# Optimization experiments

Hardware: AMD Instinct MI355X
Metric: run time of the kernel (lower is better)

The kernel has to match this reference:

```python
import jax, jax.numpy as jnp
import numpy as np

B, D, N = 65536, 512, 1024  # batch, latent_dim, som_dim**2


def setup_inputs() -> dict:
    key = jax.random.key(0)
    k1, k2, k3, k4, k5 = jax.random.split(key, 5)
    return {
        "x": jax.random.normal(k1, (B, D), dtype=jnp.float32),
        "W": jax.random.normal(k2, (D, D), dtype=jnp.float32) * 0.02,
        "b": jax.random.normal(k3, (D,), dtype=jnp.float32) * 0.02,
        "prototypes": jax.random.normal(k4, (N, D), dtype=jnp.float32),
        "temp_raw": jnp.array([0.5], dtype=jnp.float32),
    }


def reference(x, W, b, prototypes, temp_raw):
    # encoder_fc: Linear(latent_dim, latent_dim)
    z = x @ W.T + b  # [B, D]
    # torch.cdist (p=2) via ||z||^2 + ||p||^2 - 2 z.p, avoids [B,N,D] intermediate
    z_sq = jnp.sum(z * z, axis=-1, keepdims=True)          # [B, 1]
    p_sq = jnp.sum(prototypes * prototypes, axis=-1)        # [N]
    d2 = jnp.maximum(z_sq + p_sq - 2.0 * (z @ prototypes.T), 1e-12)
    dists = jnp.sqrt(d2)                                    # [B, N]
    # temperature = sigmoid(temp_raw) * (1 - 0.001) + 0.001
    temp = jax.nn.sigmoid(temp_raw[0]) * (1.0 - 0.001) + 0.001
    weights = jax.nn.softmax(-dists / temp, axis=-1)        # [B, N]
    blended = weights @ prototypes                          # [B, D]
    return blended, weights
```

## Files before the change

kernel.cpp:

```cpp
#include <hip/hip_runtime.h>

#define DDIM 512
#define NPROT 1024

typedef float fvec4 __attribute__((ext_vector_type(4)));
typedef __bf16 bf16x8 __attribute__((ext_vector_type(8)));
typedef unsigned short us4 __attribute__((ext_vector_type(4)));
typedef unsigned short us8 __attribute__((ext_vector_type(8)));
typedef __attribute__((address_space(1))) unsigned int gu32;
typedef __attribute__((address_space(3))) unsigned int lu32;

__device__ __forceinline__ unsigned short f2bf(float f) {
  unsigned u = __float_as_uint(f);
  u += 0x7fffu + ((u >> 16) & 1u);
  return (unsigned short)(u >> 16);
}
__device__ __forceinline__ float bf2f(unsigned short h) {
  return __uint_as_float(((unsigned)h) << 16);
}
__device__ __forceinline__ void gl_lds16(const void* g, void* l) {
  __builtin_amdgcn_global_load_lds((gu32*)(unsigned long long)g,
                                   (lu32*)(unsigned)(unsigned long long)l,
                                   16, 0, 0);
}

__global__ __launch_bounds__(256) void prep_kernel(
    const float* __restrict__ W, const float* __restrict__ P,
    unsigned short* __restrict__ Wb, unsigned short* __restrict__ Pb,
    unsigned short* __restrict__ PTb, float* __restrict__ psq) {
  __shared__ float tile[32][33];
  const int b = blockIdx.x;
  const int t = threadIdx.x;
  if (b < 256) {
    int e = (b * 256 + t) * 4;
    fvec4 v = *(const fvec4*)(W + e);
    us4 o; o.x = f2bf(v.x); o.y = f2bf(v.y); o.z = f2bf(v.z); o.w = f2bf(v.w);
    *(us4*)(Wb + e) = o;
  } else if (b < 768) {
    int e = ((b - 256) * 256 + t) * 4;
    fvec4 v = *(const fvec4*)(P + e);
    us4 o; o.x = f2bf(v.x); o.y = f2bf(v.y); o.z = f2bf(v.z); o.w = f2bf(v.w);
    *(us4*)(Pb + e) = o;
  } else if (b < 1280) {
    int rel = b - 768;
    int d0 = (rel >> 5) * 32;
    int n0 = (rel & 31) * 32;
    int r = t >> 3;
    int c4 = (t & 7) * 4;
    fvec4 v = *(const fvec4*)(P + (size_t)(n0 + r) * DDIM + d0 + c4);
    tile[r][c4 + 0] = v.x; tile[r][c4 + 1] = v.y;
    tile[r][c4 + 2] = v.z; tile[r][c4 + 3] = v.w;
    __syncthreads();
    us4 o;
    o.x = f2bf(tile[c4 + 0][r]);
    o.y = f2bf(tile[c4 + 1][r]);
    o.z = f2bf(tile[c4 + 2][r]);
    o.w = f2bf(tile[c4 + 3][r]);
    *(us4*)(PTb + (size_t)(d0 + r) * NPROT + n0 + c4) = o;
  } else {
    int l = t & 63;
    int row = (b - 1280) * 4 + (t >> 6);
    const float* pr = P + (size_t)row * DDIM;
    fvec4 a = *(const fvec4*)(pr + l * 4);
    fvec4 c = *(const fvec4*)(pr + 256 + l * 4);
    float s = a.x * a.x + a.y * a.y + a.z * a.z + a.w * a.w +
              c.x * c.x + c.y * c.y + c.z * c.z + c.w * c.w;
    for (int o = 32; o > 0; o >>= 1) s += __shfl_xor(s, o);
    if (l == 0) psq[row] = s;
  }
}

__global__ __launch_bounds__(256) void g1_kernel(
    const float* __restrict__ x, const unsigned short* __restrict__ Wb,
    const float* __restrict__ bias, unsigned short* __restrict__ z) {
  __shared__ unsigned short Ab[128 * 32];
  __shared__ unsigned short Bb[128 * 32];
  const int t = threadIdx.x;
  const int bm = blockIdx.x, bn = blockIdx.y;
  const int w = t >> 6, l = t & 63, lr = l & 15, lq = l >> 4;
  const int wm = (w >> 1) * 64, wn = (w & 1) * 64;
  fvec4 acc[4][4];
#pragma unroll
  for (int r = 0; r < 4; r++)
#pragma unroll
    for (int c = 0; c < 4; c++) acc[r][c] = 0.0f;
  const float* Ag = x + (size_t)bm * 128 * DDIM;
  const unsigned short* Bg = Wb + (size_t)bn * 128 * DDIM;
  for (int k0 = 0; k0 < DDIM; k0 += 32) {
    __syncthreads();
#pragma unroll
    for (int i = 0; i < 2; i++) {
      int c = i * 256 + t;
      gl_lds16(Bg + (size_t)(c >> 2) * DDIM + k0 + (c & 3) * 8, Bb + c * 8);
    }
#pragma unroll
    for (int i = 0; i < 4; i++) {
      int c = i * 256 + t;
      int row = c >> 3, j = (c & 7) * 4;
      fvec4 v = *(const fvec4*)(Ag + (size_t)row * DDIM + k0 + j);
      us4 o; o.x = f2bf(v.x); o.y = f2bf(v.y); o.z = f2bf(v.z); o.w = f2bf(v.w);
      *(us4*)(Ab + row * 32 + j) = o;
    }
    __syncthreads();
    bf16x8 af[4], bfr[4];
#pragma unroll
    for (int r = 0; r < 4; r++)
      af[r] = *(const bf16x8*)(Ab + (wm + r * 16 + lr) * 32 + lq * 8);
#pragma unroll
    for (int c = 0; c < 4; c++)
      bfr[c] = *(const bf16x8*)(Bb + (wn + c * 16 + lr) * 32 + lq * 8);
#pragma unroll
    for (int r = 0; r < 4; r++)
#pragma unroll
      for (int c = 0; c < 4; c++)
        acc[r][c] = __builtin_amdgcn_mfma_f32_16x16x32_bf16(af[r], bfr[c], acc[r][c], 0, 0, 0);
  }
  const int rbase = bm * 128 + wm + lq * 4;
  const int cbase = bn * 128 + wn + lr;
#pragma unroll
  for (int c = 0; c < 4; c++) {
    int col = cbase + c * 16;
    float bc = bias[col];
#pragma unroll
    for (int r = 0; r < 4; r++) {
      int row = rbase + r * 16;
#pragma unroll
      for (int v = 0; v < 4; v++)
        z[(size_t)(row + v) * DDIM + col] = f2bf(acc[r][c][v] + bc);
    }
  }
}

__global__ __launch_bounds__(256) void zsq_kernel(
    const unsigned short* __restrict__ z, float* __restrict__ zsq) {
  const int t = threadIdx.x, l = t & 63;
  const size_t row = (size_t)blockIdx.x * 4 + (t >> 6);
  us8 u = *(const us8*)(z + row * DDIM + l * 8);
  float s = 0.f;
#pragma unroll
  for (int i = 0; i < 8; i++) { float f = bf2f(u[i]); s += f * f; }
  for (int o = 32; o > 0; o >>= 1) s += __shfl_xor(s, o);
  if (l == 0) zsq[row] = s;
}

__global__ __launch_bounds__(256) void g2_kernel(
    const unsigned short* __restrict__ z, const unsigned short* __restrict__ Pb,
    const float* __restrict__ zsq, const float* __restrict__ psq,
    const float* __restrict__ temp_raw, float* __restrict__ logits) {
  __shared__ unsigned short Ab[128 * 32];
  __shared__ unsigned short Bb[128 * 32];
  const int t = threadIdx.x;
  const int bm = blockIdx.x, bn = blockIdx.y;
  const int w = t >> 6, l = t & 63, lr = l & 15, lq = l >> 4;
  const int wm = (w >> 1) * 64, wn = (w & 1) * 64;
  fvec4 acc[4][4];
#pragma unroll
  for (int r = 0; r < 4; r++)
#pragma unroll
    for (int c = 0; c < 4; c++) acc[r][c] = 0.0f;
  const unsigned short* Ag = z + (size_t)bm * 128 * DDIM;
  const unsigned short* Bg = Pb + (size_t)bn * 128 * DDIM;
  for (int k0 = 0; k0 < DDIM; k0 += 32) {
    __syncthreads();
#pragma unroll
    for (int i = 0; i < 2; i++) {
      int c = i * 256 + t;
      gl_lds16(Ag + (size_t)(c >> 2) * DDIM + k0 + (c & 3) * 8, Ab + c * 8);
      gl_lds16(Bg + (size_t)(c >> 2) * DDIM + k0 + (c & 3) * 8, Bb + c * 8);
    }
    __syncthreads();
    bf16x8 af[4], bfr[4];
#pragma unroll
    for (int r = 0; r < 4; r++)
      af[r] = *(const bf16x8*)(Ab + (wm + r * 16 + lr) * 32 + lq * 8);
#pragma unroll
    for (int c = 0; c < 4; c++)
      bfr[c] = *(const bf16x8*)(Bb + (wn + c * 16 + lr) * 32 + lq * 8);
#pragma unroll
    for (int r = 0; r < 4; r++)
#pragma unroll
      for (int c = 0; c < 4; c++)
        acc[r][c] = __builtin_amdgcn_mfma_f32_16x16x32_bf16(af[r], bfr[c], acc[r][c], 0, 0, 0);
  }
  const float temp = 0.999f / (1.0f + __expf(-temp_raw[0])) + 0.001f;
  const float nit = -1.0f / temp;
  const int rbase = bm * 128 + wm + lq * 4;
  const int cbase = bn * 128 + wn + lr;
  float zr[4][4];
#pragma unroll
  for (int r = 0; r < 4; r++)
#pragma unroll
    for (int v = 0; v < 4; v++) zr[r][v] = zsq[rbase + r * 16 + v];
#pragma unroll
  for (int c = 0; c < 4; c++) {
    int col = cbase + c * 16;
    float pc = psq[col];
#pragma unroll
    for (int r = 0; r < 4; r++)
#pragma unroll
      for (int v = 0; v < 4; v++) {
        float d2 = fmaxf(zr[r][v] + pc - 2.0f * acc[r][c][v], 1e-12f);
        logits[(size_t)(rbase + r * 16 + v) * NPROT + col] = nit * sqrtf(d2);
      }
  }
}

__global__ __launch_bounds__(256) void softmax_kernel(float* __restrict__ wio) {
  const int t = threadIdx.x, l = t & 63;
  float* p = wio + ((size_t)blockIdx.x * 4 + (t >> 6)) * NPROT;
  fvec4 v[4];
#pragma unroll
  for (int j = 0; j < 4; j++) v[j] = *(const fvec4*)(p + (j * 64 + l) * 4);
  float m = -3.4e38f;
#pragma unroll
  for (int j = 0; j < 4; j++)
    m = fmaxf(m, fmaxf(fmaxf(v[j].x, v[j].y), fmaxf(v[j].z, v[j].w)));
  for (int o = 32; o > 0; o >>= 1) m = fmaxf(m, __shfl_xor(m, o));
  float s = 0.f;
#pragma unroll
  for (int j = 0; j < 4; j++) {
    v[j].x = __expf(v[j].x - m); v[j].y = __expf(v[j].y - m);
    v[j].z = __expf(v[j].z - m); v[j].w = __expf(v[j].w - m);
    s += v[j].x + v[j].y + v[j].z + v[j].w;
  }
  for (int o = 32; o > 0; o >>= 1) s += __shfl_xor(s, o);
  const float rinv = 1.0f / s;
#pragma unroll
  for (int j = 0; j < 4; j++) {
    v[j] *= rinv;
    *(fvec4*)(p + (j * 64 + l) * 4) = v[j];
  }
}

__global__ __launch_bounds__(256) void g3_kernel(
    const float* __restrict__ wgt, const unsigned short* __restrict__ PTb,
    float* __restrict__ blended) {
  __shared__ unsigned short Ab[128 * 32];
  __shared__ unsigned short Bb[128 * 32];
  const int t = threadIdx.x;
  const int bm = blockIdx.x, bn = blockIdx.y;
  const int w = t >> 6, l = t & 63, lr = l & 15, lq = l >> 4;
  const int wm = (w >> 1) * 64, wn = (w & 1) * 64;
  fvec4 acc[4][4];
#pragma unroll
  for (int r = 0; r < 4; r++)
#pragma unroll
    for (int c = 0; c < 4; c++) acc[r][c] = 0.0f;
  const float* Ag = wgt + (size_t)bm * 128 * NPROT;
  const unsigned short* Bg = PTb + (size_t)bn * 128 * NPROT;
  for (int k0 = 0; k0 < NPROT; k0 += 32) {
    __syncthreads();
#pragma unroll
    for (int i = 0; i < 2; i++) {
      int c = i * 256 + t;
      gl_lds16(Bg + (size_t)(c >> 2) * NPROT + k0 + (c & 3) * 8, Bb + c * 8);
    }
#pragma unroll
    for (int i = 0; i < 4; i++) {
      int c = i * 256 + t;
      int row = c >> 3, j = (c & 7) * 4;
      fvec4 v = *(const fvec4*)(Ag + (size_t)row * NPROT + k0 + j);
      us4 o; o.x = f2bf(v.x); o.y = f2bf(v.y); o.z = f2bf(v.z); o.w = f2bf(v.w);
      *(us4*)(Ab + row * 32 + j) = o;
    }
    __syncthreads();
    bf16x8 af[4], bfr[4];
#pragma unroll
    for (int r = 0; r < 4; r++)
      af[r] = *(const bf16x8*)(Ab + (wm + r * 16 + lr) * 32 + lq * 8);
#pragma unroll
    for (int c = 0; c < 4; c++)
      bfr[c] = *(const bf16x8*)(Bb + (wn + c * 16 + lr) * 32 + lq * 8);
#pragma unroll
    for (int r = 0; r < 4; r++)
#pragma unroll
      for (int c = 0; c < 4; c++)
        acc[r][c] = __builtin_amdgcn_mfma_f32_16x16x32_bf16(af[r], bfr[c], acc[r][c], 0, 0, 0);
  }
  const int rbase = bm * 128 + wm + lq * 4;
  const int cbase = bn * 128 + wn + lr;
#pragma unroll
  for (int c = 0; c < 4; c++) {
    int col = cbase + c * 16;
#pragma unroll
    for (int r = 0; r < 4; r++) {
      int row = rbase + r * 16;
#pragma unroll
      for (int v = 0; v < 4; v++)
        blended[(size_t)(row + v) * DDIM + col] = acc[r][c][v];
    }
  }
}

extern "C" void kernel_launch(void* const* d_in, const int* in_sizes, int n_in,
                              void* d_out, int out_size, void* d_ws, size_t ws_size,
                              hipStream_t stream) {
  (void)in_sizes; (void)n_in; (void)out_size; (void)ws_size;
  const float* x  = (const float*)d_in[0];
  const float* W  = (const float*)d_in[1];
  const float* bv = (const float*)d_in[2];
  const float* P  = (const float*)d_in[3];
  const float* tr = (const float*)d_in[4];

  float* out = (float*)d_out;
  float* blended = out;
  float* weights = out + (size_t)65536 * DDIM;
  unsigned short* zbuf = (unsigned short*)d_out;

  char* ws = (char*)d_ws;
  unsigned short* Wb  = (unsigned short*)(ws + 0);
  unsigned short* Pb  = (unsigned short*)(ws + 524288);
  unsigned short* PTb = (unsigned short*)(ws + 1572864);
  float* psq = (float*)(ws + 2621440);
  float* zsq = (float*)(ws + 2625536);

  prep_kernel<<<dim3(1536), 256, 0, stream>>>(W, P, Wb, Pb, PTb, psq);
  g1_kernel<<<dim3(512, 4), 256, 0, stream>>>(x, Wb, bv, zbuf);
  zsq_kernel<<<dim3(16384), 256, 0, stream>>>(zbuf, zsq);
  g2_kernel<<<dim3(512, 8), 256, 0, stream>>>(zbuf, Pb, zsq, psq, tr, weights);
  softmax_kernel<<<dim3(16384), 256, 0, stream>>>(weights);
  g3_kernel<<<dim3(512, 4), 256, 0, stream>>>(weights, PTb, blended);
}
```

Before: 971.8 us.

## Widen g3 tile to full output width and swizzle g1/g2 block order

g3 now uses 512-thread blocks that each compute a 128x512 tile covering the whole output width. Each fp32 weight row tile is read from global memory and converted to bf16 once, instead of once for each of the 4 column blocks. g1 and g2 switch to a 1D grid in which consecutive blocks share the same row tile, so the A rows can be reused from L2. In exchange g3 uses more registers per thread (32 accumulators) and larger LDS, and launches only 512 blocks, which may lower occupancy.

```diff
diff --git a/kernel.cpp b/kernel.cpp
--- a/kernel.cpp
+++ b/kernel.cpp
@@ -76,7 +76,8 @@
   __shared__ unsigned short Ab[128 * 32];
   __shared__ unsigned short Bb[128 * 32];
   const int t = threadIdx.x;
-  const int bm = blockIdx.x, bn = blockIdx.y;
+  const int bi = blockIdx.x;
+  const int bm = bi >> 2, bn = bi & 3;
   const int w = t >> 6, l = t & 63, lr = l & 15, lq = l >> 4;
   const int wm = (w >> 1) * 64, wn = (w & 1) * 64;
   fvec4 acc[4][4];
@@ -150,7 +151,8 @@
   __shared__ unsigned short Ab[128 * 32];
   __shared__ unsigned short Bb[128 * 32];
   const int t = threadIdx.x;
-  const int bm = blockIdx.x, bn = blockIdx.y;
+  const int bi = blockIdx.x;
+  const int bm = bi >> 3, bn = bi & 7;
   const int w = t >> 6, l = t & 63, lr = l & 15, lq = l >> 4;
   const int wm = (w >> 1) * 64, wn = (w & 1) * 64;
   fvec4 acc[4][4];
@@ -232,56 +234,57 @@
   }
 }
 
-__global__ __launch_bounds__(256) void g3_kernel(
+__global__ __launch_bounds__(512) void g3_kernel(
     const float* __restrict__ wgt, const unsigned short* __restrict__ PTb,
     float* __restrict__ blended) {
   __shared__ unsigned short Ab[128 * 32];
-  __shared__ unsigned short Bb[128 * 32];
+  __shared__ unsigned short Bb[512 * 32];
   const int t = threadIdx.x;
-  const int bm = blockIdx.x, bn = blockIdx.y;
+  const int bm = blockIdx.x;
   const int w = t >> 6, l = t & 63, lr = l & 15, lq = l >> 4;
-  const int wm = (w >> 1) * 64, wn = (w & 1) * 64;
-  fvec4 acc[4][4];
+  const int wm = (w >> 2) * 64;
+  const int wn = (w & 3) * 128;
+  fvec4 acc[4][8];
 #pragma unroll
   for (int r = 0; r < 4; r++)
 #pragma unroll
-    for (int c = 0; c < 4; c++) acc[r][c] = 0.0f;
+    for (int c = 0; c < 8; c++) acc[r][c] = 0.0f;
   const float* Ag = wgt + (size_t)bm * 128 * NPROT;
-  const unsigned short* Bg = PTb + (size_t)bn * 128 * NPROT;
   for (int k0 = 0; k0 < NPROT; k0 += 32) {
     __syncthreads();
 #pragma unroll
-    for (int i = 0; i < 2; i++) {
-      int c = i * 256 + t;
-      gl_lds16(Bg + (size_t)(c >> 2) * NPROT + k0 + (c & 3) * 8, Bb + c * 8);
-    }
-#pragma unroll
     for (int i = 0; i < 4; i++) {
-      int c = i * 256 + t;
-      int row = c >> 3, j = (c & 7) * 4;
-      fvec4 v = *(const fvec4*)(Ag + (size_t)row * NPROT + k0 + j);
-      us4 o; o.x = f2bf(v.x); o.y = f2bf(v.y); o.z = f2bf(v.z); o.w = f2bf(v.w);
-      *(us4*)(Ab + row * 32 + j) = o;
-    }
-    __syncthreads();
-    bf16x8 af[4], bfr[4];
+      int c = i * 512 + t;
+      gl_lds16(PTb + (size_t)(c >> 2) * NPROT + k0 + (c & 3) * 8, Bb + c * 8);
+    }
+    {
+      int row = t >> 2, j = (t & 3) * 8;
+      const float* src = Ag + (size_t)row * NPROT + k0 + j;
+      fvec4 v0 = *(const fvec4*)(src);
+      fvec4 v1 = *(const fvec4*)(src + 4);
+      us8 o;
+      o[0] = f2bf(v0.x); o[1] = f2bf(v0.y); o[2] = f2bf(v0.z); o[3] = f2bf(v0.w);
+      o[4] = f2bf(v1.x); o[5] = f2bf(v1.y); o[6] = f2bf(v1.z); o[7] = f2bf(v1.w);
+      *(us8*)(Ab + row * 32 + j) = o;
+    }
+    __syncthreads();
+    bf16x8 af[4], bfr[8];
 #pragma unroll
     for (int r = 0; r < 4; r++)
       af[r] = *(const bf16x8*)(Ab + (wm + r * 16 + lr) * 32 + lq * 8);
 #pragma unroll
-    for (int c = 0; c < 4; c++)
+    for (int c = 0; c < 8; c++)
       bfr[c] = *(const bf16x8*)(Bb + (wn + c * 16 + lr) * 32 + lq * 8);
 #pragma unroll
     for (int r = 0; r < 4; r++)
 #pragma unroll
-      for (int c = 0; c < 4; c++)
+      for (int c = 0; c < 8; c++)
         acc[r][c] = __builtin_amdgcn_mfma_f32_16x16x32_bf16(af[r], bfr[c], acc[r][c], 0, 0, 0);
   }
   const int rbase = bm * 128 + wm + lq * 4;
-  const int cbase = bn * 128 + wn + lr;
-#pragma unroll
-  for (int c = 0; c < 4; c++) {
-    int col = cbase + c * 16;
+#pragma unroll
+  for (int c = 0; c < 8; c++) {
+    int col = wn + c * 16 + lr;
 #pragma unroll
     for (int r = 0; r < 4; r++) {
       int row = rbase + r * 16;
@@ -315,9 +318,9 @@
   float* zsq = (float*)(ws + 2625536);
 
   prep_kernel<<<dim3(1536), 256, 0, stream>>>(W, P, Wb, Pb, PTb, psq);
-  g1_kernel<<<dim3(512, 4), 256, 0, stream>>>(x, Wb, bv, zbuf);
+  g1_kernel<<<dim3(2048), 256, 0, stream>>>(x, Wb, bv, zbuf);
   zsq_kernel<<<dim3(16384), 256, 0, stream>>>(zbuf, zsq);
-  g2_kernel<<<dim3(512, 8), 256, 0, stream>>>(zbuf, Pb, zsq, psq, tr, weights);
+  g2_kernel<<<dim3(4096), 256, 0, stream>>>(zbuf, Pb, zsq, psq, tr, weights);
   softmax_kernel<<<dim3(16384), 256, 0, stream>>>(weights);
-  g3_kernel<<<dim3(512, 4), 256, 0, stream>>>(weights, PTb, blended);
-}
+  g3_kernel<<<dim3(512), 512, 0, stream>>>(weights, PTb, blended);
+}
```

After: 908.2 us. 1.07x faster.
